# Kernel optimization log

Hardware: AMD Instinct MI355X
Metric: run time of the kernel (lower is better)

## Reference

```python
import jax, jax.numpy as jnp
import numpy as np

N, M, DZ, DX, HEADS = 8192, 128, 128, 128, 4


def setup_inputs() -> dict:
    key = jax.random.key(0)
    k1, k2, k3 = jax.random.split(key, 3)
    z = jax.random.normal(k1, (N, DZ), dtype=jnp.float32)
    x = jax.random.normal(k2, (DX, M), dtype=jnp.float32)
    # MLP([input_size, heads]) -> single Linear(DZ+DX, HEADS) + final_act
    W = jax.random.normal(k3, (DZ + DX, HEADS), dtype=jnp.float32) * (1.0 / np.sqrt(DZ + DX))
    b = jnp.zeros((HEADS,), dtype=jnp.float32)
    return {"z": z, "x": x, "W": W, "b": b}


def reference(z, x, W, b):
    # Original: cat([repeat_interleave(z[:,None], M, 1), x.T.repeat(N,1,1)], -1) @ W + b
    # Fused equivalent: split W into the z-part and x-part and broadcast-add.
    dz = z.shape[1]
    zW = jnp.einsum('nd,dh->nh', z, W[:dz])        # [N, H]
    xW = jnp.einsum('dm,dh->mh', x, W[dz:])        # [M, H] (x.T @ W2)
    out = zW[:, None, :] + xW[None, :, :] + b      # [N, M, H]
    return jax.nn.relu(out)
```

## Files before the change

### kernel.cpp

```cpp
#include <hip/hip_runtime.h>


union F4 { float4 v; float f[4]; };

__device__ __forceinline__ int sw(int r) { return r + (r >> 3); }

__global__ void __launch_bounds__(256) gam_stage1(
    const float* __restrict__ z, const float* __restrict__ x,
    const float* __restrict__ W, const float* __restrict__ b,
    float4* __restrict__ zw_ws, float4* __restrict__ t_ws)
{
    __shared__ float4 Wf[292];
    __shared__ float4 tpart[2][128];

    const int t   = threadIdx.x;
    const int blk = blockIdx.x;

    const float4* zp = (const float4*)(z + (size_t)blk * 16 * 128);
    F4 a0, a1;
    a0.v = zp[t];
    a1.v = zp[t + 256];

    Wf[sw(t)] = ((const float4*)W)[t];
    __syncthreads();

    {
        const int d0 = (t & 31) * 4;
        float4 p0 = make_float4(0.f,0.f,0.f,0.f);
        float4 p1 = make_float4(0.f,0.f,0.f,0.f);
#pragma unroll
        for (int j = 0; j < 4; ++j) {
            float4 w = Wf[sw(d0 + j)];
            p0.x = fmaf(a0.f[j], w.x, p0.x); p0.y = fmaf(a0.f[j], w.y, p0.y);
            p0.z = fmaf(a0.f[j], w.z, p0.z); p0.w = fmaf(a0.f[j], w.w, p0.w);
            p1.x = fmaf(a1.f[j], w.x, p1.x); p1.y = fmaf(a1.f[j], w.y, p1.y);
            p1.z = fmaf(a1.f[j], w.z, p1.z); p1.w = fmaf(a1.f[j], w.w, p1.w);
        }
#pragma unroll
        for (int off = 16; off; off >>= 1) {
            p0.x += __shfl_xor(p0.x, off); p0.y += __shfl_xor(p0.y, off);
            p0.z += __shfl_xor(p0.z, off); p0.w += __shfl_xor(p0.w, off);
            p1.x += __shfl_xor(p1.x, off); p1.y += __shfl_xor(p1.y, off);
            p1.z += __shfl_xor(p1.z, off); p1.w += __shfl_xor(p1.w, off);
        }
        if ((t & 31) == 0) {
            const int r = t >> 5;
            zw_ws[blk * 16 + r]     = p0;
            zw_ws[blk * 16 + r + 8] = p1;
        }
    }

    if (blk == 0) {
        const int m    = t & 127;
        const int half = t >> 7;
        const float* xp = x + (size_t)(half * 64) * 128 + m;
        float4 acc = make_float4(0.f, 0.f, 0.f, 0.f);
#pragma unroll 8
        for (int dd = 0; dd < 64; ++dd) {
            float  xv = xp[dd * 128];
            float4 w  = Wf[sw(128 + half * 64 + dd)];
            acc.x = fmaf(xv, w.x, acc.x);
            acc.y = fmaf(xv, w.y, acc.y);
            acc.z = fmaf(xv, w.z, acc.z);
            acc.w = fmaf(xv, w.w, acc.w);
        }
        tpart[half][m] = acc;
        __syncthreads();
        if (t < 128) {
            float4 bv = *(const float4*)b;
            float4 q0 = tpart[0][t];
            float4 q1 = tpart[1][t];
            float4 tv;
            tv.x = q0.x + q1.x + bv.x;
            tv.y = q0.y + q1.y + bv.y;
            tv.z = q0.z + q1.z + bv.z;
            tv.w = q0.w + q1.w + bv.w;
            t_ws[t] = tv;
        }
    }
}

__global__ void __launch_bounds__(256) gam_stage2(
    const float4* __restrict__ zw_ws, const float4* __restrict__ t_ws,
    float4* __restrict__ out4)
{
    const int t   = threadIdx.x;
    const int blk = blockIdx.x;
    const float4  tq = t_ws[t & 127];
    const float4* zb = zw_ws + (size_t)blk * 8;
    float4* op = out4 + (size_t)blk * 1024;
#pragma unroll
    for (int it = 0; it < 4; ++it) {
        const int row = it * 2 + (t >> 7);
        float4 s = zb[row];
        float4 v;
        v.x = fmaxf(tq.x + s.x, 0.f);
        v.y = fmaxf(tq.y + s.y, 0.f);
        v.z = fmaxf(tq.z + s.z, 0.f);
        v.w = fmaxf(tq.w + s.w, 0.f);
        op[it * 256 + t] = v;
    }
}

extern "C" void kernel_launch(void* const* d_in, const int* in_sizes, int n_in,
                              void* d_out, int out_size, void* d_ws, size_t ws_size,
                              hipStream_t stream) {
    const float* z = (const float*)d_in[0];
    const float* x = (const float*)d_in[1];
    const float* W = (const float*)d_in[2];
    const float* b = (const float*)d_in[3];
    float4* zw_ws = (float4*)d_ws;
    float4* t_ws  = (float4*)d_ws + 8192;
    gam_stage1<<<512, 256, 0, stream>>>(z, x, W, b, zw_ws, t_ws);
    gam_stage2<<<1024, 256, 0, stream>>>(zw_ws, t_ws, (float4*)d_out);
}
```

Baseline: 70.76 us.

## Fuse projection and broadcast stages into one kernel, recomputing xW per block

Merges the two kernels into a single launch. Each block computes its 8 zW rows and redundantly recomputes the full x·W2 vector plus bias in shared memory, then writes its output tile directly. This removes the second launch and the workspace round trip, at the cost of every block re-reading x (64KB) and repeating the x projection arithmetic.

```diff
diff --git a/kernel.cpp b/kernel.cpp
--- a/kernel.cpp
+++ b/kernel.cpp
@@ -5,52 +5,26 @@
 
 __device__ __forceinline__ int sw(int r) { return r + (r >> 3); }
 
-__global__ void __launch_bounds__(256) gam_stage1(
+__global__ void __launch_bounds__(256) gam_fused(
     const float* __restrict__ z, const float* __restrict__ x,
     const float* __restrict__ W, const float* __restrict__ b,
-    float4* __restrict__ zw_ws, float4* __restrict__ t_ws)
+    float4* __restrict__ out4)
 {
     __shared__ float4 Wf[292];
     __shared__ float4 tpart[2][128];
+    __shared__ float4 tvec[128];
+    __shared__ float4 zw[8];
 
     const int t   = threadIdx.x;
     const int blk = blockIdx.x;
 
-    const float4* zp = (const float4*)(z + (size_t)blk * 16 * 128);
-    F4 a0, a1;
-    a0.v = zp[t];
-    a1.v = zp[t + 256];
+    const float4* zp = (const float4*)(z + (size_t)blk * 8 * 128);
+    F4 a0; a0.v = zp[t];
 
     Wf[sw(t)] = ((const float4*)W)[t];
     __syncthreads();
 
     {
-        const int d0 = (t & 31) * 4;
-        float4 p0 = make_float4(0.f,0.f,0.f,0.f);
-        float4 p1 = make_float4(0.f,0.f,0.f,0.f);
-#pragma unroll
-        for (int j = 0; j < 4; ++j) {
-            float4 w = Wf[sw(d0 + j)];
-            p0.x = fmaf(a0.f[j], w.x, p0.x); p0.y = fmaf(a0.f[j], w.y, p0.y);
-            p0.z = fmaf(a0.f[j], w.z, p0.z); p0.w = fmaf(a0.f[j], w.w, p0.w);
-            p1.x = fmaf(a1.f[j], w.x, p1.x); p1.y = fmaf(a1.f[j], w.y, p1.y);
-            p1.z = fmaf(a1.f[j], w.z, p1.z); p1.w = fmaf(a1.f[j], w.w, p1.w);
-        }
-#pragma unroll
-        for (int off = 16; off; off >>= 1) {
-            p0.x += __shfl_xor(p0.x, off); p0.y += __shfl_xor(p0.y, off);
-            p0.z += __shfl_xor(p0.z, off); p0.w += __shfl_xor(p0.w, off);
-            p1.x += __shfl_xor(p1.x, off); p1.y += __shfl_xor(p1.y, off);
-            p1.z += __shfl_xor(p1.z, off); p1.w += __shfl_xor(p1.w, off);
-        }
-        if ((t & 31) == 0) {
-            const int r = t >> 5;
-            zw_ws[blk * 16 + r]     = p0;
-            zw_ws[blk * 16 + r + 8] = p1;
-        }
-    }
-
-    if (blk == 0) {
         const int m    = t & 127;
         const int half = t >> 7;
         const float* xp = x + (size_t)(half * 64) * 128 + m;
@@ -65,40 +39,57 @@
             acc.w = fmaf(xv, w.w, acc.w);
         }
         tpart[half][m] = acc;
-        __syncthreads();
-        if (t < 128) {
-            float4 bv = *(const float4*)b;
-            float4 q0 = tpart[0][t];
-            float4 q1 = tpart[1][t];
-            float4 tv;
-            tv.x = q0.x + q1.x + bv.x;
-            tv.y = q0.y + q1.y + bv.y;
-            tv.z = q0.z + q1.z + bv.z;
-            tv.w = q0.w + q1.w + bv.w;
-            t_ws[t] = tv;
+    }
+
+    {
+        const int d0 = (t & 31) * 4;
+        float4 p0 = make_float4(0.f, 0.f, 0.f, 0.f);
+#pragma unroll
+        for (int j = 0; j < 4; ++j) {
+            float4 w = Wf[sw(d0 + j)];
+            p0.x = fmaf(a0.f[j], w.x, p0.x);
+            p0.y = fmaf(a0.f[j], w.y, p0.y);
+            p0.z = fmaf(a0.f[j], w.z, p0.z);
+            p0.w = fmaf(a0.f[j], w.w, p0.w);
         }
+#pragma unroll
+        for (int off = 16; off; off >>= 1) {
+            p0.x += __shfl_xor(p0.x, off);
+            p0.y += __shfl_xor(p0.y, off);
+            p0.z += __shfl_xor(p0.z, off);
+            p0.w += __shfl_xor(p0.w, off);
+        }
+        if ((t & 31) == 0) zw[t >> 5] = p0;
     }
-}
+    __syncthreads();
 
-__global__ void __launch_bounds__(256) gam_stage2(
-    const float4* __restrict__ zw_ws, const float4* __restrict__ t_ws,
-    float4* __restrict__ out4)
-{
-    const int t   = threadIdx.x;
-    const int blk = blockIdx.x;
-    const float4  tq = t_ws[t & 127];
-    const float4* zb = zw_ws + (size_t)blk * 8;
-    float4* op = out4 + (size_t)blk * 1024;
+    if (t < 128) {
+        float4 bv = *(const float4*)b;
+        float4 q0 = tpart[0][t];
+        float4 q1 = tpart[1][t];
+        float4 tv;
+        tv.x = q0.x + q1.x + bv.x;
+        tv.y = q0.y + q1.y + bv.y;
+        tv.z = q0.z + q1.z + bv.z;
+        tv.w = q0.w + q1.w + bv.w;
+        tvec[t] = tv;
+    }
+    __syncthreads();
+
+    {
+        const float4 tq = tvec[t & 127];
+        float4* op = out4 + (size_t)blk * 1024;
 #pragma unroll
-    for (int it = 0; it < 4; ++it) {
-        const int row = it * 2 + (t >> 7);
-        float4 s = zb[row];
-        float4 v;
-        v.x = fmaxf(tq.x + s.x, 0.f);
-        v.y = fmaxf(tq.y + s.y, 0.f);
-        v.z = fmaxf(tq.z + s.z, 0.f);
-        v.w = fmaxf(tq.w + s.w, 0.f);
-        op[it * 256 + t] = v;
+        for (int it = 0; it < 4; ++it) {
+            const int row = it * 2 + (t >> 7);
+            float4 s = zw[row];
+            float4 v;
+            v.x = fmaxf(tq.x + s.x, 0.f);
+            v.y = fmaxf(tq.y + s.y, 0.f);
+            v.z = fmaxf(tq.z + s.z, 0.f);
+            v.w = fmaxf(tq.w + s.w, 0.f);
+            op[it * 256 + t] = v;
+        }
     }
 }
 
@@ -109,8 +100,5 @@
     const float* x = (const float*)d_in[1];
     const float* W = (const float*)d_in[2];
     const float* b = (const float*)d_in[3];
-    float4* zw_ws = (float4*)d_ws;
-    float4* t_ws  = (float4*)d_ws + 8192;
-    gam_stage1<<<512, 256, 0, stream>>>(z, x, W, b, zw_ws, t_ws);
-    gam_stage2<<<1024, 256, 0, stream>>>(zw_ws, t_ws, (float4*)d_out);
+    gam_fused<<<1024, 256, 0, stream>>>(z, x, W, b, (float4*)d_out);
 }
```

After: 69.53 us. About the same (-1.7%).
